# Performance work log

Measured on AMD Instinct MI355X. Metric: run time of the kernel, lower is better.

The kernel has to match this reference:

```python
import jax, jax.numpy as jnp
import numpy as np

DIM = 384
D_STATE = 16


def setup_inputs() -> dict:
    key = jax.random.key(0)
    ks = jax.random.split(key, 8)
    B, C, H, W = 4, DIM, 64, 64
    x = jax.random.normal(ks[0], (B, C, H, W), dtype=jnp.float32)
    P = 2 * DIM + 2 * D_STATE  # proj output width
    W_proj = jax.random.normal(ks[1], (P, DIM), dtype=jnp.float32) * 0.02
    b_proj = jnp.zeros((P,), dtype=jnp.float32)
    # A_log = log(uniform(0,1) + 1e-4) as in torch init
    A_log = jnp.log(jax.random.uniform(ks[2], (DIM, D_STATE), dtype=jnp.float32) + 1e-4)
    D = jnp.ones((DIM,), dtype=jnp.float32)
    dt_bias = jnp.zeros((DIM,), dtype=jnp.float32)
    W_out = jax.random.normal(ks[3], (DIM, DIM), dtype=jnp.float32) * 0.02
    b_out = jnp.zeros((DIM,), dtype=jnp.float32)
    return {"x": x, "W_proj": W_proj, "b_proj": b_proj, "A_log": A_log,
            "D": D, "dt_bias": dt_bias, "W_out": W_out, "b_out": b_out}


def _selective_scan(x_in, delta, A, Bm, Cm, D):
    # x_in, delta: (B, L, dim); Bm, Cm: (B, L, n); A: (dim, n); D: (dim,)
    Bsz, L, dim = x_in.shape
    n = A.shape[1]

    def step(h, inp):
        d_t, x_t, b_t, c_t = inp  # (B,dim),(B,dim),(B,n),(B,n)
        # h: (B, dim, n)
        h = jnp.exp(d_t[..., None] * A) * h + (d_t * x_t)[..., None] * b_t[:, None, :]
        y_t = jnp.einsum('bdn,bn->bd', h, c_t)
        return h, y_t

    h0 = jnp.zeros((Bsz, dim, n), dtype=x_in.dtype)
    xs = (jnp.swapaxes(delta, 0, 1), jnp.swapaxes(x_in, 0, 1),
          jnp.swapaxes(Bm, 0, 1), jnp.swapaxes(Cm, 0, 1))
    _, ys = jax.lax.scan(step, h0, xs)  # ys: (L, B, dim)
    y = jnp.swapaxes(ys, 0, 1)  # (B, L, dim)
    return y + x_in * D


def reference(x, W_proj, b_proj, A_log, D, dt_bias, W_out, b_out):
    B, C, H, W = x.shape
    L = H * W
    seq = x.reshape(B, C, L).transpose(0, 2, 1)  # (B, L, C)
    proj = seq @ W_proj.T + b_proj  # (B, L, 2*dim + 2*n)
    x_in = proj[..., :DIM]
    delta = proj[..., DIM:2 * DIM]
    Bm = proj[..., 2 * DIM:2 * DIM + D_STATE]
    Cm = proj[..., 2 * DIM + D_STATE:]
    A = -jnp.exp(A_log)  # (dim, n)
    delta = jax.nn.softplus(delta + dt_bias)  # delta_bias + delta_softplus
    y = _selective_scan(x_in, delta, A, Bm, Cm, D)  # (B, L, dim)
    out = y @ W_out.T + b_out  # (B, L, dim)
    return out.transpose(0, 2, 1).reshape(B, C, H, W)
```

## Files before the change

kernel.cpp:

```cpp
#include <hip/hip_runtime.h>
#include <cstdint>
#include <cstddef>

#define DIMC 384
#define DST  16
#define LLEN 4096
#define NB   4
#define PDIM 800
#define NCH  128
#define CL   32
#define KDIM 384

typedef __attribute__((ext_vector_type(8))) short bf16x8;
typedef __attribute__((ext_vector_type(4))) float f32x4;

#define GLOAD16(g, l) __builtin_amdgcn_global_load_lds( \
    (const __attribute__((address_space(1))) uint32_t*)(g), \
    (__attribute__((address_space(3))) uint32_t*)(l), 16, 0, 0)

__device__ __forceinline__ float softplus_f(float v) {
    if (v > 20.f) return v;
    return logf(1.f + __expf(v));
}

__device__ __forceinline__ ushort f2bf(float x) {
    uint32_t u = __float_as_uint(x);
    uint32_t r = (u + 0x7FFFu + ((u >> 16) & 1u)) >> 16;
    return (ushort)r;
}

__global__ __launch_bounds__(256)
void cast_bf(const float* __restrict__ in, ushort* __restrict__ out,
             int n_src, int n_tot)
{
    int i = (blockIdx.x * 256 + threadIdx.x) * 4;
    if (i >= n_tot) return;
    if (i < n_src) {
        float4 v = *(const float4*)(in + i);
        ushort4 s; s.x = f2bf(v.x); s.y = f2bf(v.y); s.z = f2bf(v.z); s.w = f2bf(v.w);
        *(ushort4*)(out + i) = s;
    } else {
        ushort4 s; s.x = 0; s.y = 0; s.z = 0; s.w = 0;
        *(ushort4*)(out + i) = s;
    }
}

__global__ __launch_bounds__(256)
void transpose_cast(const float* __restrict__ in, ushort* __restrict__ out)
{
    __shared__ float t[64][65];
    const int tid = threadIdx.x;
    const int b  = blockIdx.z;
    const int c0 = blockIdx.y * 64;
    const int l0 = blockIdx.x * 64;
    const float* ip = in + ((size_t)b * DIMC + c0) * LLEN + l0;
    #pragma unroll
    for (int r = 0; r < 4; ++r) {
        int cl = (tid >> 4) + r * 16;
        int l4 = (tid & 15) * 4;
        float4 v = *(const float4*)(ip + (size_t)cl * LLEN + l4);
        t[cl][l4 + 0] = v.x; t[cl][l4 + 1] = v.y;
        t[cl][l4 + 2] = v.z; t[cl][l4 + 3] = v.w;
    }
    __syncthreads();
    ushort* op = out + ((size_t)b * LLEN + l0) * DIMC + c0;
    #pragma unroll
    for (int r = 0; r < 4; ++r) {
        int ll = (tid >> 4) + r * 16;
        int c4 = (tid & 15) * 4;
        ushort4 s;
        s.x = f2bf(t[c4 + 0][ll]); s.y = f2bf(t[c4 + 1][ll]);
        s.z = f2bf(t[c4 + 2][ll]); s.w = f2bf(t[c4 + 3][ll]);
        *(ushort4*)(op + (size_t)ll * DIMC + c4) = s;
    }
}

template<int EPI>
__global__ __launch_bounds__(256)
void mfma_gemm(const ushort* __restrict__ Abf, const ushort* __restrict__ Wbf,
               const float* __restrict__ bias, const float* __restrict__ dt_bias,
               float* __restrict__ o_x, float* __restrict__ o_dt,
               float* __restrict__ o_Bm, float* __restrict__ o_Cm,
               float* __restrict__ o_out)
{
    __shared__ ushort Alds[128 * 32];
    __shared__ ushort Blds[64 * 32];

    const int tid = threadIdx.x;
    const int m0  = blockIdx.x * 128;
    const int n0  = blockIdx.y * 64;
    const int w   = tid >> 6;
    const int ln  = tid & 63;
    const int wm  = w * 32;
    const int fr  = ln & 15;
    const int fg  = ln >> 4;

    const int srow = tid >> 2;
    const int sg   = tid & 3;

    const ushort* Ag = Abf + (size_t)m0 * KDIM;
    const ushort* Bg = Wbf + (size_t)n0 * KDIM;

    f32x4 acc[2][4];
    #pragma unroll
    for (int i = 0; i < 2; ++i)
        #pragma unroll
        for (int j = 0; j < 4; ++j)
            acc[i][j] = (f32x4){0.f, 0.f, 0.f, 0.f};

    for (int k0 = 0; k0 < KDIM; k0 += 32) {
        if (k0) __syncthreads();
        {
            int a0 = sg ^ ((srow >> 1) & 3);
            GLOAD16(Ag + (size_t)srow * KDIM + k0 + a0 * 8, &Alds[tid * 8]);
            int r1 = srow + 64;
            int a1 = sg ^ ((r1 >> 1) & 3);
            GLOAD16(Ag + (size_t)r1 * KDIM + k0 + a1 * 8, &Alds[2048 + tid * 8]);
            GLOAD16(Bg + (size_t)srow * KDIM + k0 + a0 * 8, &Blds[tid * 8]);
        }
        __syncthreads();
        bf16x8 af[2], bfv[4];
        #pragma unroll
        for (int i = 0; i < 2; ++i) {
            int r = wm + i * 16 + fr;
            af[i] = *(const bf16x8*)&Alds[r * 32 + ((fg ^ ((r >> 1) & 3)) << 3)];
        }
        #pragma unroll
        for (int j = 0; j < 4; ++j) {
            int r = j * 16 + fr;
            bfv[j] = *(const bf16x8*)&Blds[r * 32 + ((fg ^ ((r >> 1) & 3)) << 3)];
        }
        #pragma unroll
        for (int i = 0; i < 2; ++i)
            #pragma unroll
            for (int j = 0; j < 4; ++j)
                acc[i][j] = __builtin_amdgcn_mfma_f32_16x16x32_bf16(af[i], bfv[j], acc[i][j], 0, 0, 0);
    }

    const int b   = m0 / LLEN;
    const int ml0 = m0 - b * LLEN;
    #pragma unroll
    for (int j = 0; j < 4; ++j) {
        const int n = n0 + j * 16 + fr;
        #pragma unroll
        for (int i = 0; i < 2; ++i) {
            const int l = ml0 + wm + i * 16 + fg * 4;
            f32x4 v = acc[i][j];
            if (EPI == 0) {
                if (n < DIMC) {
                    const float bb = bias[n];
                    float4 st; st.x = v[0] + bb; st.y = v[1] + bb; st.z = v[2] + bb; st.w = v[3] + bb;
                    *(float4*)(o_x + ((size_t)b * DIMC + n) * LLEN + l) = st;
                } else if (n < 2 * DIMC) {
                    const int d = n - DIMC;
                    const float bb = bias[n] + dt_bias[d];
                    float4 st;
                    st.x = softplus_f(v[0] + bb); st.y = softplus_f(v[1] + bb);
                    st.z = softplus_f(v[2] + bb); st.w = softplus_f(v[3] + bb);
                    *(float4*)(o_dt + ((size_t)b * DIMC + d) * LLEN + l) = st;
                } else if (n < 2 * DIMC + DST) {
                    const int s = n - 2 * DIMC;
                    const float bb = bias[n];
                    #pragma unroll
                    for (int r = 0; r < 4; ++r)
                        o_Bm[((size_t)b * LLEN + l + r) * DST + s] = v[r] + bb;
                } else if (n < PDIM) {
                    const int s = n - 2 * DIMC - DST;
                    const float bb = bias[n];
                    #pragma unroll
                    for (int r = 0; r < 4; ++r)
                        o_Cm[((size_t)b * LLEN + l + r) * DST + s] = v[r] + bb;
                }
            } else {
                const float bb = bias[n];
                float4 st; st.x = v[0] + bb; st.y = v[1] + bb; st.z = v[2] + bb; st.w = v[3] + bb;
                *(float4*)(o_out + ((size_t)b * DIMC + n) * LLEN + l) = st;
            }
        }
    }
}

__global__ __launch_bounds__(384)
void scan_part1(const float* __restrict__ dt_t, const float* __restrict__ x_t,
                const float* __restrict__ Bm, const float* __restrict__ A_log,
                float* __restrict__ Pc, float* __restrict__ Qc)
{
    __shared__ float Bs[CL][DST];
    const int d   = threadIdx.x;
    const int b   = blockIdx.x >> 7;
    const int chk = blockIdx.x & (NCH - 1);
    const int l0  = chk * CL;

    if (d < (CL * DST) / 4)
        ((float4*)&Bs[0][0])[d] =
            ((const float4*)(Bm + ((size_t)b * LLEN + l0) * DST))[d];

    float Av[DST];
    #pragma unroll
    for (int r = 0; r < 4; ++r) {
        float4 v = *(const float4*)(A_log + d * DST + r * 4);
        Av[r*4+0] = -__expf(v.x); Av[r*4+1] = -__expf(v.y);
        Av[r*4+2] = -__expf(v.z); Av[r*4+3] = -__expf(v.w);
    }
    __syncthreads();

    const float* dtp = dt_t + ((size_t)b * DIMC + d) * LLEN + l0;
    const float* xp  = x_t  + ((size_t)b * DIMC + d) * LLEN + l0;

    float P[DST], q[DST];
    #pragma unroll
    for (int n = 0; n < DST; ++n) { P[n] = 1.f; q[n] = 0.f; }

    for (int t0 = 0; t0 < CL; t0 += 4) {
        float4 dt4 = *(const float4*)(dtp + t0);
        float4 x4  = *(const float4*)(xp + t0);
        float dts[4] = {dt4.x, dt4.y, dt4.z, dt4.w};
        float xs[4]  = {x4.x, x4.y, x4.z, x4.w};
        #pragma unroll
        for (int j = 0; j < 4; ++j) {
            const float dt  = dts[j];
            const float dtx = dt * xs[j];
            #pragma unroll
            for (int n = 0; n < DST; ++n) {
                float a = __expf(dt * Av[n]);
                P[n] *= a;
                q[n] = fmaf(a, q[n], dtx * Bs[t0 + j][n]);
            }
        }
    }
    const size_t o = (((size_t)b * NCH + chk) * DIMC + d) * DST;
    #pragma unroll
    for (int r = 0; r < 4; ++r) {
        *(float4*)(Pc + o + r * 4) = *(float4*)&P[r * 4];
        *(float4*)(Qc + o + r * 4) = *(float4*)&q[r * 4];
    }
}

__global__ __launch_bounds__(256)
void scan_carry(const float* __restrict__ Pc, const float* __restrict__ Qc,
                float* __restrict__ Hin)
{
    const int idx = blockIdx.x * 256 + threadIdx.x;
    const int bd  = idx >> 4;
    const int n   = idx & 15;
    const int b   = bd / DIMC;
    const int d   = bd - b * DIMC;
    float h = 0.f;
    for (int chk = 0; chk < NCH; ++chk) {
        const size_t o = (((size_t)b * NCH + chk) * DIMC + d) * DST + n;
        Hin[o] = h;
        h = fmaf(Pc[o], h, Qc[o]);
    }
}

__global__ __launch_bounds__(384)
void scan_part3(const float* __restrict__ dt_t, const float* __restrict__ x_t,
                const float* __restrict__ Bm, const float* __restrict__ Cm,
                const float* __restrict__ A_log, const float* __restrict__ Dv,
                const float* __restrict__ Hin, ushort* __restrict__ y_bfT)
{
    __shared__ float Bs[CL][DST];
    __shared__ float Cs[CL][DST];
    const int d   = threadIdx.x;
    const int b   = blockIdx.x >> 7;
    const int chk = blockIdx.x & (NCH - 1);
    const int l0  = chk * CL;

    if (d < 128)
        ((float4*)&Bs[0][0])[d] =
            ((const float4*)(Bm + ((size_t)b * LLEN + l0) * DST))[d];
    else if (d < 256)
        ((float4*)&Cs[0][0])[d - 128] =
            ((const float4*)(Cm + ((size_t)b * LLEN + l0) * DST))[d - 128];

    float Av[DST];
    #pragma unroll
    for (int r = 0; r < 4; ++r) {
        float4 v = *(const float4*)(A_log + d * DST + r * 4);
        Av[r*4+0] = -__expf(v.x); Av[r*4+1] = -__expf(v.y);
        Av[r*4+2] = -__expf(v.z); Av[r*4+3] = -__expf(v.w);
    }
    const float Dd = Dv[d];
    __syncthreads();

    float h[DST];
    const size_t ho = (((size_t)b * NCH + chk) * DIMC + d) * DST;
    #pragma unroll
    for (int r = 0; r < 4; ++r)
        *(float4*)&h[r * 4] = *(const float4*)(Hin + ho + r * 4);

    const float* dtp = dt_t + ((size_t)b * DIMC + d) * LLEN + l0;
    const float* xp  = x_t  + ((size_t)b * DIMC + d) * LLEN + l0;
    ushort* yp = y_bfT + ((size_t)b * LLEN + l0) * DIMC + d;

    for (int t0 = 0; t0 < CL; t0 += 4) {
        float4 dt4 = *(const float4*)(dtp + t0);
        float4 x4  = *(const float4*)(xp + t0);
        float dts[4] = {dt4.x, dt4.y, dt4.z, dt4.w};
        float xs[4]  = {x4.x, x4.y, x4.z, x4.w};
        #pragma unroll
        for (int j = 0; j < 4; ++j) {
            const float dt  = dts[j];
            const float xx  = xs[j];
            const float dtx = dt * xx;
            float yv = Dd * xx;
            #pragma unroll
            for (int n = 0; n < DST; ++n) {
                float a = __expf(dt * Av[n]);
                h[n] = fmaf(a, h[n], dtx * Bs[t0 + j][n]);
                yv = fmaf(h[n], Cs[t0 + j][n], yv);
            }
            yp[(size_t)(t0 + j) * DIMC] = f2bf(yv);
        }
    }
}

extern "C" void kernel_launch(void* const* d_in, const int* in_sizes, int n_in,
                              void* d_out, int out_size, void* d_ws, size_t ws_size,
                              hipStream_t stream)
{
    const float* x      = (const float*)d_in[0];
    const float* W_proj = (const float*)d_in[1];
    const float* b_proj = (const float*)d_in[2];
    const float* A_log  = (const float*)d_in[3];
    const float* Dv     = (const float*)d_in[4];
    const float* dt_b   = (const float*)d_in[5];
    const float* W_out  = (const float*)d_in[6];
    const float* b_out  = (const float*)d_in[7];
    float* out = (float*)d_out;
    float* ws  = (float*)d_ws;

    const size_t szBD = (size_t)NB * DIMC * LLEN;
    const size_t szBC = (size_t)NB * LLEN * DST;
    const size_t szPQ = (size_t)NB * NCH * DIMC * DST;
    float* x_t  = ws;
    float* dt_t = x_t + szBD;
    float* Bmw  = dt_t + szBD;
    float* Cmw  = Bmw + szBC;
    float* Pc   = Cmw + szBC;
    float* Qc   = Pc + szPQ;
    float* Hin  = Qc + szPQ;
    ushort* x_bfT = (ushort*)(Hin + szPQ);
    ushort* y_bfT = x_bfT + szBD;
    ushort* Wp_bf = y_bfT + szBD;
    ushort* Wo_bf = Wp_bf + (size_t)832 * KDIM;

    cast_bf<<<(832 * KDIM) / 1024, 256, 0, stream>>>(W_proj, Wp_bf,
                                                     PDIM * KDIM, 832 * KDIM);
    cast_bf<<<(DIMC * KDIM) / 1024, 256, 0, stream>>>(W_out, Wo_bf,
                                                      DIMC * KDIM, DIMC * KDIM);
    dim3 tg(LLEN / 64, DIMC / 64, NB);
    transpose_cast<<<tg, 256, 0, stream>>>(x, x_bfT);

    dim3 g1((NB * LLEN) / 128, (PDIM + 63) / 64);
    mfma_gemm<0><<<g1, 256, 0, stream>>>(x_bfT, Wp_bf, b_proj, dt_b,
                                         x_t, dt_t, Bmw, Cmw, nullptr);

    scan_part1<<<NB * NCH, 384, 0, stream>>>(dt_t, x_t, Bmw, A_log, Pc, Qc);
    scan_carry<<<(NB * DIMC * DST) / 256, 256, 0, stream>>>(Pc, Qc, Hin);
    scan_part3<<<NB * NCH, 384, 0, stream>>>(dt_t, x_t, Bmw, Cmw,
                                             A_log, Dv, Hin, y_bfT);

    dim3 g2((NB * LLEN) / 128, DIMC / 64);
    mfma_gemm<1><<<g2, 256, 0, stream>>>(y_bfT, Wo_bf, b_out, nullptr,
                                         nullptr, nullptr, nullptr, nullptr,
                                         out);
}
```

Before: 245.6 us.

## Store x and delta intermediates in (B, L, dim) layout for coalesced scan loads

The projection GEMM epilogue now writes x_in and softplus(delta) in (batch, time, channel) order instead of (batch, channel, time). Both scan kernels then read each timestep with neighbouring threads (channels) touching consecutive addresses, replacing per-thread float4 loads that were strided by LLEN across the wavefront. The cost moves to the GEMM epilogue, which now issues scalar stores strided by DIMC per row instead of float4 stores, and the coalescing of those stores depends on how the MFMA fragment rows map to lanes.

```diff
diff --git a/kernel.cpp b/kernel.cpp
--- a/kernel.cpp
+++ b/kernel.cpp
@@ -149,15 +149,15 @@
             if (EPI == 0) {
                 if (n < DIMC) {
                     const float bb = bias[n];
-                    float4 st; st.x = v[0] + bb; st.y = v[1] + bb; st.z = v[2] + bb; st.w = v[3] + bb;
-                    *(float4*)(o_x + ((size_t)b * DIMC + n) * LLEN + l) = st;
+                    #pragma unroll
+                    for (int r = 0; r < 4; ++r)
+                        o_x[((size_t)b * LLEN + l + r) * DIMC + n] = v[r] + bb;
                 } else if (n < 2 * DIMC) {
                     const int d = n - DIMC;
                     const float bb = bias[n] + dt_bias[d];
-                    float4 st;
-                    st.x = softplus_f(v[0] + bb); st.y = softplus_f(v[1] + bb);
-                    st.z = softplus_f(v[2] + bb); st.w = softplus_f(v[3] + bb);
-                    *(float4*)(o_dt + ((size_t)b * DIMC + d) * LLEN + l) = st;
+                    #pragma unroll
+                    for (int r = 0; r < 4; ++r)
+                        o_dt[((size_t)b * LLEN + l + r) * DIMC + d] = softplus_f(v[r] + bb);
                 } else if (n < 2 * DIMC + DST) {
                     const int s = n - 2 * DIMC;
                     const float bb = bias[n];
@@ -204,18 +204,20 @@
     }
     __syncthreads();
 
-    const float* dtp = dt_t + ((size_t)b * DIMC + d) * LLEN + l0;
-    const float* xp  = x_t  + ((size_t)b * DIMC + d) * LLEN + l0;
+    const float* dtp = dt_t + ((size_t)b * LLEN + l0) * DIMC + d;
+    const float* xp  = x_t  + ((size_t)b * LLEN + l0) * DIMC + d;
 
     float P[DST], q[DST];
     #pragma unroll
     for (int n = 0; n < DST; ++n) { P[n] = 1.f; q[n] = 0.f; }
 
     for (int t0 = 0; t0 < CL; t0 += 4) {
-        float4 dt4 = *(const float4*)(dtp + t0);
-        float4 x4  = *(const float4*)(xp + t0);
-        float dts[4] = {dt4.x, dt4.y, dt4.z, dt4.w};
-        float xs[4]  = {x4.x, x4.y, x4.z, x4.w};
+        float dts[4], xs[4];
+        #pragma unroll
+        for (int j = 0; j < 4; ++j) {
+            dts[j] = dtp[(size_t)(t0 + j) * DIMC];
+            xs[j]  = xp[(size_t)(t0 + j) * DIMC];
+        }
         #pragma unroll
         for (int j = 0; j < 4; ++j) {
             const float dt  = dts[j];
@@ -289,15 +291,17 @@
     for (int r = 0; r < 4; ++r)
         *(float4*)&h[r * 4] = *(const float4*)(Hin + ho + r * 4);
 
-    const float* dtp = dt_t + ((size_t)b * DIMC + d) * LLEN + l0;
-    const float* xp  = x_t  + ((size_t)b * DIMC + d) * LLEN + l0;
+    const float* dtp = dt_t + ((size_t)b * LLEN + l0) * DIMC + d;
+    const float* xp  = x_t  + ((size_t)b * LLEN + l0) * DIMC + d;
     ushort* yp = y_bfT + ((size_t)b * LLEN + l0) * DIMC + d;
 
     for (int t0 = 0; t0 < CL; t0 += 4) {
-        float4 dt4 = *(const float4*)(dtp + t0);
-        float4 x4  = *(const float4*)(xp + t0);
-        float dts[4] = {dt4.x, dt4.y, dt4.z, dt4.w};
-        float xs[4]  = {x4.x, x4.y, x4.z, x4.w};
+        float dts[4], xs[4];
+        #pragma unroll
+        for (int j = 0; j < 4; ++j) {
+            dts[j] = dtp[(size_t)(t0 + j) * DIMC];
+            xs[j]  = xp[(size_t)(t0 + j) * DIMC];
+        }
         #pragma unroll
         for (int j = 0; j < 4; ++j) {
             const float dt  = dts[j];
```

After: 210.3 us. 1.17x faster.
